# Performance work log

Measured on AMD Instinct MI355X. Metric: run time of the kernel, lower is better.

## Reference

```python
import jax, jax.numpy as jnp
import numpy as np

B, S, E, H = 4, 1024, 1024, 32
D = E // H  # head_dim == num_heads (required by phase broadcast in original code)


def setup_inputs() -> dict:
    key = jax.random.key(0)
    ks = jax.random.split(key, 20)
    s = 0.02
    inp = {
        "x": jax.random.normal(ks[0], (B, S, E), jnp.float32),
        # q/k/v projections (torch Linear: y = x @ W.T + b)
        "q_w": jax.random.normal(ks[1], (E, E), jnp.float32) * s,
        "q_b": jnp.zeros((E,), jnp.float32),
        "k_w": jax.random.normal(ks[2], (E, E), jnp.float32) * s,
        "k_b": jnp.zeros((E,), jnp.float32),
        "v_w": jax.random.normal(ks[3], (E, E), jnp.float32) * s,
        "v_b": jnp.zeros((E,), jnp.float32),
        # phase encoder: Linear(E,E) -> ReLU -> Linear(E,H)
        "ph_w1": jax.random.normal(ks[4], (E, E), jnp.float32) * s,
        "ph_b1": jnp.zeros((E,), jnp.float32),
        "ph_w2": jax.random.normal(ks[5], (H, E), jnp.float32) * s,
        "ph_b2": jnp.zeros((H,), jnp.float32),
        # nn.MultiheadAttention params (packed in_proj + out_proj)
        "in_proj_w": jax.random.normal(ks[6], (3 * E, E), jnp.float32) * s,
        "in_proj_b": jnp.zeros((3 * E,), jnp.float32),
        "out_proj_w": jax.random.normal(ks[7], (E, E), jnp.float32) * s,
        "out_proj_b": jnp.zeros((E,), jnp.float32),
        # final output projection
        "final_w": jax.random.normal(ks[8], (E, E), jnp.float32) * s,
        "final_b": jnp.zeros((E,), jnp.float32),
    }
    return inp


def _heads(t):  # (B,S,E) -> (B,H,S,D)
    return t.reshape(B, S, H, D).transpose(0, 2, 1, 3)


def _mha(x, in_proj_w, in_proj_b, out_proj_w, out_proj_b):
    # torch nn.MultiheadAttention self-attention, batch_first=True, no mask
    qkv = x @ in_proj_w.T + in_proj_b  # (B,S,3E)
    q, k, v = jnp.split(qkv, 3, axis=-1)
    q, k, v = _heads(q), _heads(k), _heads(v)
    scores = jnp.einsum("bhqd,bhkd->bhqk", q, k) / jnp.sqrt(jnp.float32(D))
    attn = jax.nn.softmax(scores, axis=-1)
    ctx = jnp.einsum("bhqk,bhkd->bhqd", attn, v)
    ctx = ctx.transpose(0, 2, 1, 3).reshape(B, S, E)
    return ctx @ out_proj_w.T + out_proj_b


def reference(x, q_w, q_b, k_w, k_b, v_w, v_b, ph_w1, ph_b1, ph_w2, ph_b2,
              in_proj_w, in_proj_b, out_proj_w, out_proj_b, final_w, final_b):
    Q = _heads(x @ q_w.T + q_b)  # (B,H,S,D)
    K = _heads(x @ k_w.T + k_b)
    V = _heads(x @ v_w.T + v_b)

    # phase: (B,H) -> cos -> broadcast over last (head_dim) axis, D == H
    h = jax.nn.relu(jnp.mean(x, axis=1) @ ph_w1.T + ph_b1)
    phase = jnp.cos(h @ ph_w2.T + ph_b2)  # (B,H)
    phase = phase[:, None, None, :]  # (B,1,1,H) multiplies head_dim axis

    Q = Q * phase
    K = K * phase
    scores = jnp.einsum("bhqd,bhkd->bhqk", Q, K) / jnp.sqrt(jnp.float32(D))
    attn_weights = jax.nn.softmax(scores, axis=-1)  # (B,H,S,S)
    context = jnp.einsum("bhqk,bhkd->bhqd", attn_weights, V)
    context = context.transpose(0, 2, 1, 3).reshape(B, S, E)

    entangled = _mha(context, in_proj_w, in_proj_b, out_proj_w, out_proj_b)
    output = (entangled + context) @ final_w.T + final_b
    return output, attn_weights
```

## Files before the change

### kernel.cpp

```cpp
#include <hip/hip_runtime.h>
#include <hip/hip_bf16.h>
#include <cstdint>
#include <cstddef>

typedef __bf16 bf16_t;
typedef __bf16 bf16x8 __attribute__((ext_vector_type(8)));
typedef __bf16 bf16x4 __attribute__((ext_vector_type(4)));
typedef float  f32x4  __attribute__((ext_vector_type(4)));

static constexpr int Bb = 4, Ss = 1024, Ee = 1024, Hh = 32, Dd = 32;
static constexpr int Ntok = Bb * Ss;
static constexpr int E3   = 3 * Ee;
static constexpr float SCALE = 0.17677669529663687f;

__device__ __forceinline__ void gl_lds16(const void* g, void* l) {
  __builtin_amdgcn_global_load_lds(
      (const __attribute__((address_space(1))) void*)g,
      (__attribute__((address_space(3))) void*)l, 16, 0, 0);
}

__global__ __launch_bounds__(256) void conv_all(const float* __restrict__ x,  const float* __restrict__ qw,
                                                const float* __restrict__ kw, const float* __restrict__ vw,
                                                const float* __restrict__ inw,const float* __restrict__ ow,
                                                const float* __restrict__ fw,
                                                bf16_t* xb, bf16_t* qb, bf16_t* kb, bf16_t* vb,
                                                bf16_t* inb, bf16_t* ob, bf16_t* fb) {
  const int i = blockIdx.x * 256 + threadIdx.x;
  const float* src; bf16_t* dst; int base;
  if      (i < 1048576) { src = x;   dst = xb;  base = 0; }
  else if (i < 1310720) { src = qw;  dst = qb;  base = 1048576; }
  else if (i < 1572864) { src = kw;  dst = kb;  base = 1310720; }
  else if (i < 1835008) { src = vw;  dst = vb;  base = 1572864; }
  else if (i < 2621440) { src = inw; dst = inb; base = 1835008; }
  else if (i < 2883584) { src = ow;  dst = ob;  base = 2621440; }
  else                  { src = fw;  dst = fb;  base = 2883584; }
  const int j = i - base;
  const float4 v = *(const float4*)(src + (size_t)j * 4);
  bf16x4 o = {(bf16_t)v.x, (bf16_t)v.y, (bf16_t)v.z, (bf16_t)v.w};
  *(bf16x4*)(dst + (size_t)j * 4) = o;
}

__global__ __launch_bounds__(256) void prepb(const float* __restrict__ qb, const float* __restrict__ kb,
                                             const float* __restrict__ vb, float* __restrict__ o) {
  const int i = blockIdx.x * 256 + threadIdx.x;
  o[i] = (i < 1024) ? qb[i] : (i < 2048) ? kb[i - 1024] : vb[i - 2048];
}

__global__ __launch_bounds__(256) void biasck(const float* __restrict__ fw, const float* __restrict__ ob,
                                              const float* __restrict__ fb, float* __restrict__ bc) {
  const int t = threadIdx.x;
  const int n = blockIdx.x * 64 + (t >> 2), p = t & 3;
  const float* row = fw + (size_t)n * 1024 + p * 256;
  const float* obp = ob + p * 256;
  float s = 0.f;
  for (int j = 0; j < 256; ++j) s += row[j] * obp[j];
  s += __shfl_xor(s, 1);
  s += __shfl_xor(s, 2);
  if (p == 0) bc[n] = s + fb[n];
}

__global__ __launch_bounds__(256) void colmean_part(const float* __restrict__ x,
                                                    float* __restrict__ part) {
  const int b = blockIdx.y, sc = blockIdx.x;
  const float* base = x + ((size_t)b * Ss + sc * 32) * Ee;
  for (int k = 0; k < 4; ++k) {
    const int e = threadIdx.x + k * 256;
    float s = 0.f;
    for (int i = 0; i < 32; ++i) s += base[(size_t)i * Ee + e];
    part[((size_t)sc * 4 + b) * Ee + e] = s;
  }
}
__global__ __launch_bounds__(256) void colmean_fin(const float* __restrict__ part,
                                                   float* __restrict__ xm) {
  const int idx = blockIdx.x * 256 + threadIdx.x;
  const int b = idx >> 10, e = idx & 1023;
  float s = 0.f;
  for (int sc = 0; sc < 32; ++sc) s += part[((size_t)sc * 4 + b) * Ee + e];
  xm[idx] = s * (1.0f / 1024.0f);
}

__global__ __launch_bounds__(256) void hgemm(const float* __restrict__ xm,
                                             const float* __restrict__ w1,
                                             const float* __restrict__ b1,
                                             float* __restrict__ hout) {
  __shared__ float xl[4 * 1024];
  for (int i = threadIdx.x; i < 4096; i += 256) xl[i] = xm[i];
  __syncthreads();
  const int j = blockIdx.x * 64 + (threadIdx.x >> 2);
  const int b = threadIdx.x & 3;
  const float* wr = w1 + (size_t)j * Ee;
  const float* xr = xl + b * 1024;
  float s = 0.f;
  for (int e = 0; e < 1024; ++e) s += xr[e] * wr[e];
  s += b1[j];
  hout[b * 1024 + j] = fmaxf(s, 0.f);
}

__global__ __launch_bounds__(128) void phasek(const float* __restrict__ hin,
                                              const float* __restrict__ w2,
                                              const float* __restrict__ b2,
                                              float* __restrict__ ph) {
  const int t = threadIdx.x;
  const int b = t >> 5, hh = t & 31;
  const float* hr = hin + b * 1024;
  const float* wr = w2 + (size_t)hh * Ee;
  float s = 0.f;
  for (int j = 0; j < 1024; ++j) s += hr[j] * wr[j];
  ph[t] = cosf(s + b2[hh]);
}

__global__ __launch_bounds__(256) void transpose1024(const bf16_t* __restrict__ in,
                                                     bf16_t* __restrict__ out) {
  __shared__ bf16_t t[64][72];
  const int jt = threadIdx.x >> 2, k16 = (threadIdx.x & 3) * 16;
  const int r0 = blockIdx.y * 64, c0 = blockIdx.x * 64;
  const bf16x8 a = *(const bf16x8*)(in + (size_t)(r0 + jt) * 1024 + c0 + k16);
  const bf16x8 b = *(const bf16x8*)(in + (size_t)(r0 + jt) * 1024 + c0 + k16 + 8);
  *(bf16x8*)&t[jt][k16] = a;
  *(bf16x8*)&t[jt][k16 + 8] = b;
  __syncthreads();
  bf16x8 v0, v1;
#pragma unroll
  for (int m = 0; m < 8; ++m) v0[m] = t[k16 + m][jt];
#pragma unroll
  for (int m = 0; m < 8; ++m) v1[m] = t[k16 + 8 + m][jt];
  *(bf16x8*)(out + (size_t)(c0 + jt) * 1024 + r0 + k16) = v0;
  *(bf16x8*)(out + (size_t)(c0 + jt) * 1024 + r0 + k16 + 8) = v1;
}

template <int MODE>
__global__ __launch_bounds__(256) void gemm_bt(const bf16_t* __restrict__ A,
                                               const bf16_t* __restrict__ A2,
                                               const bf16_t* __restrict__ Bt,
                                               const bf16_t* __restrict__ Bt2,
                                               const float* __restrict__ bias,
                                               void* __restrict__ Cout,
                                               const float* __restrict__ phase,
                                               int K, int lda, int ldb, int ldc) {
  __shared__ bf16_t As[128 * 32];
  __shared__ bf16_t Bs[128 * 32];
  const int tid = threadIdx.x;
  const int w = tid >> 6, lane = tid & 63;
  const int nwg = gridDim.x * gridDim.y;
  int flat = blockIdx.y * gridDim.x + blockIdx.x;
  flat = (flat & 7) * (nwg >> 3) + (flat >> 3);
  const int m0 = (flat / gridDim.x) * 128, n0 = (flat % gridDim.x) * 128;
  const int wr = (w >> 1) * 64, wc = (w & 1) * 64;
  const int r_ld = lane >> 2, c_ld = (lane & 3) * 8;
  const int rr = lane & 15, kk8 = (lane >> 4) * 8;
  f32x4 acc[4][4];
#pragma unroll
  for (int m = 0; m < 4; ++m)
#pragma unroll
    for (int n = 0; n < 4; ++n) acc[m][n] = f32x4{0.f, 0.f, 0.f, 0.f};

  for (int kt = 0; kt < K; kt += 32) {
    const bf16_t* Ak = A;
    const bf16_t* Bk = Bt;
    int kk = kt;
    if constexpr (MODE == 5) {
      if (kt >= 1024) { Ak = A2; Bk = Bt2; kk = kt - 1024; }
    }
#pragma unroll
    for (int j = 0; j < 2; ++j) {
      const int r0 = w * 16 + j * 64;
      gl_lds16(Ak + (size_t)(m0 + r0 + r_ld) * lda + kk + c_ld, &As[r0 * 32]);
      gl_lds16(Bk + (size_t)(n0 + r0 + r_ld) * ldb + kk + c_ld, &Bs[r0 * 32]);
    }
    __syncthreads();
    bf16x8 af[4], bfr[4];
#pragma unroll
    for (int m = 0; m < 4; ++m) af[m] = *(const bf16x8*)&As[(wr + m * 16 + rr) * 32 + kk8];
#pragma unroll
    for (int n = 0; n < 4; ++n) bfr[n] = *(const bf16x8*)&Bs[(wc + n * 16 + rr) * 32 + kk8];
#pragma unroll
    for (int m = 0; m < 4; ++m)
#pragma unroll
      for (int n = 0; n < 4; ++n)
        acc[m][n] = __builtin_amdgcn_mfma_f32_16x16x32_bf16(af[m], bfr[n], acc[m][n], 0, 0, 0);
    __syncthreads();
  }

  const int rr4 = (lane >> 4) * 4, cc = lane & 15;
#pragma unroll
  for (int m = 0; m < 4; ++m) {
#pragma unroll
    for (int n = 0; n < 4; ++n) {
      const int gr0 = m0 + wr + m * 16 + rr4;
      const int gc = n0 + wc + n * 16 + cc;
      const float bb = bias ? bias[gc] : 0.f;
#pragma unroll
      for (int i = 0; i < 4; ++i) {
        const size_t idx = (size_t)(gr0 + i) * ldc + gc;
        float v = acc[m][n][i] + bb;
        if constexpr (MODE == 4) {
          if (gc < 2048) v *= phase[(((gr0 + i) >> 10) << 5) + ((gc >> 5) & 31)];
        }
        if constexpr (MODE == 3 || MODE == 5) ((float*)Cout)[idx] = v;
        else ((bf16_t*)Cout)[idx] = (bf16_t)v;
      }
    }
  }
}

static constexpr int K_PLANE_B = 16400;
static constexpr int V_OFF_B   = 4 * K_PLANE_B;
static constexpr int V_ROW_B   = 2064;
static constexpr int P_OFF_B   = V_OFF_B + 32 * V_ROW_B;
static constexpr int P_WAVE_B  = 2304;
static constexpr int ATTN_LDS  = P_OFF_B + 8 * P_WAVE_B;

template <int WRITE_P>
__global__ __launch_bounds__(512) void attn_fused(const bf16_t* __restrict__ Qm,
                                                  const bf16_t* __restrict__ Km, int rs,
                                                  const bf16_t* __restrict__ Vt,
                                                  float* __restrict__ Pout,
                                                  bf16_t* __restrict__ ctx, float scale) {
  extern __shared__ char smem[];
  char* Kl = smem;
  char* Vl = smem + V_OFF_B;
  const int tid = threadIdx.x, lane = tid & 63, w = tid >> 6;
  const int g = lane >> 4, r = lane & 15;
  int flat = blockIdx.y * 8 + blockIdx.x;
  flat = (flat & 7) * 128 + (flat >> 3);
  const int bh = flat >> 3, xb = flat & 7;
  const int b = bh >> 5, h = bh & 31;
  char* myP = smem + P_OFF_B + w * P_WAVE_B;

  {
    const bf16_t* Kbase = Km + (size_t)b * Ss * rs + h * 32;
    const int pg = w >> 1, hh = w & 1;
#pragma unroll
    for (int c = 0; c < 8; ++c) {
      const int row0 = hh * 512 + c * 64;
      gl_lds16(Kbase + (size_t)(row0 + lane) * rs + pg * 8, Kl + pg * K_PLANE_B + row0 * 16);
    }
  }
  {
    const bf16_t* vsrc = Vt + (size_t)bh * (Dd * Ss);
#pragma unroll
    for (int rr2 = 0; rr2 < 4; ++rr2) {
      const int row = w * 4 + rr2;
#pragma unroll
      for (int c = 0; c < 2; ++c)
        gl_lds16(vsrc + (size_t)row * Ss + c * 512 + lane * 8, Vl + row * V_ROW_B + c * 1024);
    }
  }
  const int qrow0 = xb * 128 + w * 16;
  const bf16_t* Qbase = Qm + (size_t)b * Ss * rs + h * 32;
  const bf16x8 qraw = *(const bf16x8*)(Qbase + (size_t)(qrow0 + r) * rs + g * 8);
  bf16x8 qf;
#pragma unroll
  for (int i = 0; i < 8; ++i) qf[i] = (bf16_t)((float)qraw[i] * scale);
  __syncthreads();

  const f32x4 zero = {0.f, 0.f, 0.f, 0.f};
  float lsum = 0.f;
  float rinv = 1.f;

  if constexpr (WRITE_P) {
    for (int kt = 0; kt < 16; ++kt) {
#pragma unroll
      for (int n = 0; n < 4; ++n) {
        const int key = kt * 64 + n * 16 + r;
        const bf16x8 kf = *(const bf16x8*)(Kl + g * K_PLANE_B + key * 16);
        const f32x4 s = __builtin_amdgcn_mfma_f32_16x16x32_bf16(kf, qf, zero, 0, 0, 0);
#pragma unroll
        for (int i = 0; i < 4; ++i) lsum += __expf(fminf(s[i], 60.f));
      }
    }
    lsum += __shfl_xor(lsum, 16);
    lsum += __shfl_xor(lsum, 32);
    rinv = 1.0f / lsum;
  }

  f32x4 acc2[2] = {zero, zero};
  const size_t pbase = (size_t)bh * Ss * Ss;

  for (int kt = 0; kt < 16; ++kt) {
    float p[4][4];
#pragma unroll
    for (int n = 0; n < 4; ++n) {
      const int key = kt * 64 + n * 16 + r;
      const bf16x8 kf = *(const bf16x8*)(Kl + g * K_PLANE_B + key * 16);
      const f32x4 s = __builtin_amdgcn_mfma_f32_16x16x32_bf16(kf, qf, zero, 0, 0, 0);
#pragma unroll
      for (int i = 0; i < 4; ++i) {
        float e = __expf(fminf(s[i], 60.f));
        if constexpr (WRITE_P) e *= rinv;
        else lsum += e;
        p[n][i] = e;
      }
      bf16x4 pw = {(bf16_t)p[n][0], (bf16_t)p[n][1], (bf16_t)p[n][2], (bf16_t)p[n][3]};
      *(bf16x4*)(myP + r * 144 + (n * 16 + g * 4) * 2) = pw;
      if constexpr (WRITE_P) {
        f32x4 w4 = {p[n][0], p[n][1], p[n][2], p[n][3]};
        *(f32x4*)&Pout[pbase + (size_t)(qrow0 + r) * Ss + kt * 64 + n * 16 + 4 * g] = w4;
      }
    }
#pragma unroll
    for (int c = 0; c < 2; ++c) {
      const bf16x8 pa = *(const bf16x8*)(myP + r * 144 + (c * 32 + 8 * g) * 2);
#pragma unroll
      for (int dn = 0; dn < 2; ++dn) {
        const bf16x8 vf = *(const bf16x8*)(Vl + (dn * 16 + r) * V_ROW_B +
                                           (kt * 64 + c * 32 + g * 8) * 2);
        acc2[dn] = __builtin_amdgcn_mfma_f32_16x16x32_bf16(vf, pa, acc2[dn], 0, 0, 0);
      }
    }
  }

  if constexpr (!WRITE_P) {
    lsum += __shfl_xor(lsum, 16);
    lsum += __shfl_xor(lsum, 32);
    rinv = 1.0f / lsum;
#pragma unroll
    for (int dn = 0; dn < 2; ++dn)
#pragma unroll
      for (int i = 0; i < 4; ++i) acc2[dn][i] *= rinv;
  }

  float* Ct = (float*)myP;
#pragma unroll
  for (int dn = 0; dn < 2; ++dn)
#pragma unroll
    for (int i = 0; i < 4; ++i)
      Ct[r * 36 + dn * 16 + 4 * g + i] = acc2[dn][i];
  const int q2 = lane >> 2, pt = lane & 3;
  const f32x4 ca = *(const f32x4*)(myP + q2 * 144 + pt * 32);
  const f32x4 cb = *(const f32x4*)(myP + q2 * 144 + pt * 32 + 16);
  bf16x8 cv = {(bf16_t)ca[0], (bf16_t)ca[1], (bf16_t)ca[2], (bf16_t)ca[3],
               (bf16_t)cb[0], (bf16_t)cb[1], (bf16_t)cb[2], (bf16_t)cb[3]};
  *(bf16x8*)&ctx[((size_t)b * Ss + qrow0 + q2) * Ee + h * 32 + pt * 8] = cv;
}

__global__ __launch_bounds__(256) void transpose_v(const bf16_t* __restrict__ src, int rs,
                                                   bf16_t* __restrict__ dst) {
  __shared__ bf16_t buf[128 * 33];
  const int bh = blockIdx.y, b = bh >> 5, h = bh & 31;
  const int s0 = blockIdx.x * 128;
  const bf16_t* in = src + ((size_t)b * Ss + s0) * rs + h * 32;
  for (int e = threadIdx.x; e < 128 * 32; e += 256) {
    const int s = e >> 5, d = e & 31;
    buf[s * 33 + d] = in[(size_t)s * rs + d];
  }
  __syncthreads();
  bf16_t* out = dst + (size_t)bh * (Dd * Ss) + s0;
  for (int e = threadIdx.x; e < 128 * 32; e += 256) {
    const int d = e >> 7, s = e & 127;
    out[(size_t)d * Ss + s] = buf[s * 33 + d];
  }
}

extern "C" void kernel_launch(void* const* d_in, const int* in_sizes, int n_in,
                              void* d_out, int out_size, void* d_ws, size_t ws_size,
                              hipStream_t stream) {
  const float* x     = (const float*)d_in[0];
  const float* q_w   = (const float*)d_in[1];
  const float* q_b   = (const float*)d_in[2];
  const float* k_w   = (const float*)d_in[3];
  const float* k_b   = (const float*)d_in[4];
  const float* v_w   = (const float*)d_in[5];
  const float* v_b   = (const float*)d_in[6];
  const float* ph_w1 = (const float*)d_in[7];
  const float* ph_b1 = (const float*)d_in[8];
  const float* ph_w2 = (const float*)d_in[9];
  const float* ph_b2 = (const float*)d_in[10];
  const float* in_w  = (const float*)d_in[11];
  const float* in_b  = (const float*)d_in[12];
  const float* out_w = (const float*)d_in[13];
  const float* out_b = (const float*)d_in[14];
  const float* fin_w = (const float*)d_in[15];
  const float* fin_b = (const float*)d_in[16];

  float* outp = (float*)d_out;
  float* attn_out = outp + (size_t)Ntok * Ee;

  char* ws = (char*)d_ws;
  size_t off = 0;
  auto alloc = [&](size_t bytes) -> void* {
    void* p = ws + off;
    off += (bytes + 255) & ~(size_t)255;
    return p;
  };
  bf16_t* x_bf  = (bf16_t*)alloc((size_t)Ntok * Ee * 2);
  bf16_t* wqkv  = (bf16_t*)alloc((size_t)E3 * Ee * 2);
  bf16_t* win   = (bf16_t*)alloc((size_t)E3 * Ee * 2);
  bf16_t* wout  = (bf16_t*)alloc((size_t)Ee * Ee * 2);
  bf16_t* wfin  = (bf16_t*)alloc((size_t)Ee * Ee * 2);
  bf16_t* woutT = (bf16_t*)alloc((size_t)Ee * Ee * 2);
  bf16_t* Wc    = (bf16_t*)alloc((size_t)Ee * Ee * 2);
  bf16_t* QKVb  = (bf16_t*)alloc((size_t)Ntok * E3 * 2);
  bf16_t* Vt    = (bf16_t*)alloc((size_t)Bb * Hh * Dd * Ss * 2);
  bf16_t* ctx   = (bf16_t*)alloc((size_t)Ntok * Ee * 2);
  bf16_t* qkv2  = (bf16_t*)alloc((size_t)Ntok * E3 * 2);
  bf16_t* v2t   = (bf16_t*)alloc((size_t)Bb * Hh * Dd * Ss * 2);
  bf16_t* ctx2  = (bf16_t*)alloc((size_t)Ntok * Ee * 2);
  float* part   = (float*)alloc((size_t)32 * 4 * 1024 * 4);
  float* xmean  = (float*)alloc(4096 * 4);
  float* hb     = (float*)alloc(4096 * 4);
  float* phase  = (float*)alloc(128 * 4);
  float* qkvb   = (float*)alloc(3072 * 4);
  float* bias_c = (float*)alloc(1024 * 4);

  hipFuncSetAttribute((const void*)attn_fused<1>,
                      hipFuncAttributeMaxDynamicSharedMemorySize, ATTN_LDS);
  hipFuncSetAttribute((const void*)attn_fused<0>,
                      hipFuncAttributeMaxDynamicSharedMemorySize, ATTN_LDS);

  conv_all<<<12288, 256, 0, stream>>>(x, q_w, k_w, v_w, in_w, out_w, fin_w,
                                      x_bf, wqkv, wqkv + (size_t)Ee * Ee,
                                      wqkv + (size_t)2 * Ee * Ee, win, wout, wfin);
  prepb<<<12, 256, 0, stream>>>(q_b, k_b, v_b, qkvb);
  biasck<<<16, 256, 0, stream>>>(fin_w, out_b, fin_b, bias_c);

  colmean_part<<<dim3(32, 4), 256, 0, stream>>>(x, part);
  colmean_fin<<<16, 256, 0, stream>>>(part, xmean);
  hgemm<<<16, 256, 0, stream>>>(xmean, ph_w1, ph_b1, hb);
  phasek<<<1, 128, 0, stream>>>(hb, ph_w2, ph_b2, phase);

  transpose1024<<<dim3(16, 16), 256, 0, stream>>>(wout, woutT);
  gemm_bt<0><<<dim3(8, 8), 256, 0, stream>>>(wfin, nullptr, woutT, nullptr, nullptr,
                                             Wc, nullptr, 1024, Ee, Ee, Ee);

  gemm_bt<4><<<dim3(24, 32), 256, 0, stream>>>(x_bf, nullptr, wqkv, nullptr, qkvb,
                                               QKVb, phase, 1024, Ee, Ee, E3);
  transpose_v<<<dim3(8, 128), 256, 0, stream>>>(QKVb + 2048, E3, Vt);

  attn_fused<1><<<dim3(8, 128), 512, ATTN_LDS, stream>>>(QKVb, QKVb + 1024, E3, Vt,
                                                         attn_out, ctx, SCALE);

  gemm_bt<0><<<dim3(24, 32), 256, 0, stream>>>(ctx, nullptr, win, nullptr, in_b,
                                               qkv2, nullptr, 1024, Ee, Ee, E3);
  transpose_v<<<dim3(8, 128), 256, 0, stream>>>(qkv2 + 2048, E3, v2t);
  attn_fused<0><<<dim3(8, 128), 512, ATTN_LDS, stream>>>(qkv2, qkv2 + 1024, E3, v2t,
                                                         nullptr, ctx2, SCALE);

  gemm_bt<5><<<dim3(8, 32), 256, 0, stream>>>(ctx2, ctx, Wc, wfin, bias_c,
                                              outp, nullptr, 2048, Ee, Ee, Ee);
}
```

Before: 542.2 us.

## Fuse prep kernels, reorganize K into MFMA-fragment layout, swizzle LDS, use exp2

Result: slower. 718.5 us (+32.5%).

```diff
diff --git a/kernel.cpp b/kernel.cpp
--- a/kernel.cpp
+++ b/kernel.cpp
@@ -11,7 +11,8 @@
 static constexpr int Bb = 4, Ss = 1024, Ee = 1024, Hh = 32, Dd = 32;
 static constexpr int Ntok = Bb * Ss;
 static constexpr int E3   = 3 * Ee;
-static constexpr float SCALE = 0.17677669529663687f;
+static constexpr float SCALE  = 0.17677669529663687f;
+static constexpr float SCALE2 = 0.25506060570135506f;
 
 __device__ __forceinline__ void gl_lds16(const void* g, void* l) {
   __builtin_amdgcn_global_load_lds(
@@ -19,94 +20,99 @@
       (__attribute__((address_space(3))) void*)l, 16, 0, 0);
 }
 
-__global__ __launch_bounds__(256) void conv_all(const float* __restrict__ x,  const float* __restrict__ qw,
-                                                const float* __restrict__ kw, const float* __restrict__ vw,
-                                                const float* __restrict__ inw,const float* __restrict__ ow,
-                                                const float* __restrict__ fw,
-                                                bf16_t* xb, bf16_t* qb, bf16_t* kb, bf16_t* vb,
-                                                bf16_t* inb, bf16_t* ob, bf16_t* fb) {
-  const int i = blockIdx.x * 256 + threadIdx.x;
-  const float* src; bf16_t* dst; int base;
-  if      (i < 1048576) { src = x;   dst = xb;  base = 0; }
-  else if (i < 1310720) { src = qw;  dst = qb;  base = 1048576; }
-  else if (i < 1572864) { src = kw;  dst = kb;  base = 1310720; }
-  else if (i < 1835008) { src = vw;  dst = vb;  base = 1572864; }
-  else if (i < 2621440) { src = inw; dst = inb; base = 1835008; }
-  else if (i < 2883584) { src = ow;  dst = ob;  base = 2621440; }
-  else                  { src = fw;  dst = fb;  base = 2883584; }
-  const int j = i - base;
-  const float4 v = *(const float4*)(src + (size_t)j * 4);
-  bf16x4 o = {(bf16_t)v.x, (bf16_t)v.y, (bf16_t)v.z, (bf16_t)v.w};
-  *(bf16x4*)(dst + (size_t)j * 4) = o;
-}
-
-__global__ __launch_bounds__(256) void prepb(const float* __restrict__ qb, const float* __restrict__ kb,
-                                             const float* __restrict__ vb, float* __restrict__ o) {
-  const int i = blockIdx.x * 256 + threadIdx.x;
-  o[i] = (i < 1024) ? qb[i] : (i < 2048) ? kb[i - 1024] : vb[i - 2048];
-}
-
-__global__ __launch_bounds__(256) void biasck(const float* __restrict__ fw, const float* __restrict__ ob,
-                                              const float* __restrict__ fb, float* __restrict__ bc) {
+__global__ __launch_bounds__(256) void prep(const float* __restrict__ x,  const float* __restrict__ qw,
+                                            const float* __restrict__ kw, const float* __restrict__ vw,
+                                            const float* __restrict__ inw,const float* __restrict__ ow,
+                                            const float* __restrict__ fw,
+                                            const float* __restrict__ qb, const float* __restrict__ kb,
+                                            const float* __restrict__ vb, const float* __restrict__ ob,
+                                            const float* __restrict__ fb,
+                                            bf16_t* __restrict__ xb, bf16_t* __restrict__ wqkv,
+                                            bf16_t* __restrict__ winb, bf16_t* __restrict__ wob,
+                                            bf16_t* __restrict__ wfb,
+                                            float* __restrict__ qkvb, float* __restrict__ bias_c,
+                                            float* __restrict__ part) {
+  const int bx = blockIdx.x, t = threadIdx.x;
+  if (bx < 12288) {
+    const int i = bx * 256 + t;
+    const float* src; bf16_t* dst; int base;
+    if      (i < 1048576) { src = x;   dst = xb;                       base = 0; }
+    else if (i < 1310720) { src = qw;  dst = wqkv;                     base = 1048576; }
+    else if (i < 1572864) { src = kw;  dst = wqkv + (size_t)Ee * Ee;   base = 1310720; }
+    else if (i < 1835008) { src = vw;  dst = wqkv + (size_t)2*Ee*Ee;   base = 1572864; }
+    else if (i < 2621440) { src = inw; dst = winb;                     base = 1835008; }
+    else if (i < 2883584) { src = ow;  dst = wob;                      base = 2621440; }
+    else                  { src = fw;  dst = wfb;                      base = 2883584; }
+    const int j = i - base;
+    const float4 v = *(const float4*)(src + (size_t)j * 4);
+    bf16x4 o = {(bf16_t)v.x, (bf16_t)v.y, (bf16_t)v.z, (bf16_t)v.w};
+    *(bf16x4*)(dst + (size_t)j * 4) = o;
+  } else if (bx < 12300) {
+    const int i = (bx - 12288) * 256 + t;
+    qkvb[i] = (i < 1024) ? qb[i] : (i < 2048) ? kb[i - 1024] : vb[i - 2048];
+  } else if (bx < 12316) {
+    const int n = (bx - 12300) * 64 + (t >> 2), p = t & 3;
+    const float* row = fw + (size_t)n * 1024 + p * 256;
+    const float* obp = ob + p * 256;
+    float s = 0.f;
+    for (int j = 0; j < 256; ++j) s += row[j] * obp[j];
+    s += __shfl_xor(s, 1);
+    s += __shfl_xor(s, 2);
+    if (p == 0) bias_c[n] = s + fb[n];
+  } else {
+    const int idx = bx - 12316;
+    const int sc = idx & 31, b = idx >> 5;
+    const float* base = x + ((size_t)b * Ss + sc * 32) * Ee;
+    for (int k = 0; k < 4; ++k) {
+      const int e = t + k * 256;
+      float s = 0.f;
+      for (int i = 0; i < 32; ++i) s += base[(size_t)i * Ee + e];
+      part[((size_t)sc * 4 + b) * Ee + e] = s;
+    }
+  }
+}
+
+__global__ __launch_bounds__(1024) void phase_fin(const float* __restrict__ part,
+                                                  const float* __restrict__ w1,
+                                                  const float* __restrict__ b1,
+                                                  const float* __restrict__ w2,
+                                                  const float* __restrict__ b2,
+                                                  float* __restrict__ phase) {
+  __shared__ float xm[4096];
+  __shared__ float hb[4096];
   const int t = threadIdx.x;
-  const int n = blockIdx.x * 64 + (t >> 2), p = t & 3;
-  const float* row = fw + (size_t)n * 1024 + p * 256;
-  const float* obp = ob + p * 256;
-  float s = 0.f;
-  for (int j = 0; j < 256; ++j) s += row[j] * obp[j];
-  s += __shfl_xor(s, 1);
-  s += __shfl_xor(s, 2);
-  if (p == 0) bc[n] = s + fb[n];
-}
-
-__global__ __launch_bounds__(256) void colmean_part(const float* __restrict__ x,
-                                                    float* __restrict__ part) {
-  const int b = blockIdx.y, sc = blockIdx.x;
-  const float* base = x + ((size_t)b * Ss + sc * 32) * Ee;
-  for (int k = 0; k < 4; ++k) {
-    const int e = threadIdx.x + k * 256;
+#pragma unroll
+  for (int j = 0; j < 4; ++j) {
+    const int idx = t + j * 1024;
+    const int b = idx >> 10, e = idx & 1023;
     float s = 0.f;
-    for (int i = 0; i < 32; ++i) s += base[(size_t)i * Ee + e];
-    part[((size_t)sc * 4 + b) * Ee + e] = s;
-  }
-}
-__global__ __launch_bounds__(256) void colmean_fin(const float* __restrict__ part,
-                                                   float* __restrict__ xm) {
-  const int idx = blockIdx.x * 256 + threadIdx.x;
-  const int b = idx >> 10, e = idx & 1023;
-  float s = 0.f;
-  for (int sc = 0; sc < 32; ++sc) s += part[((size_t)sc * 4 + b) * Ee + e];
-  xm[idx] = s * (1.0f / 1024.0f);
-}
-
-__global__ __launch_bounds__(256) void hgemm(const float* __restrict__ xm,
-                                             const float* __restrict__ w1,
-                                             const float* __restrict__ b1,
-                                             float* __restrict__ hout) {
-  __shared__ float xl[4 * 1024];
-  for (int i = threadIdx.x; i < 4096; i += 256) xl[i] = xm[i];
+    for (int sc = 0; sc < 32; ++sc) s += part[((size_t)sc * 4 + b) * 1024 + e];
+    xm[idx] = s * (1.0f / 1024.0f);
+  }
   __syncthreads();
-  const int j = blockIdx.x * 64 + (threadIdx.x >> 2);
-  const int b = threadIdx.x & 3;
-  const float* wr = w1 + (size_t)j * Ee;
-  const float* xr = xl + b * 1024;
-  float s = 0.f;
-  for (int e = 0; e < 1024; ++e) s += xr[e] * wr[e];
-  s += b1[j];
-  hout[b * 1024 + j] = fmaxf(s, 0.f);
-}
-
-__global__ __launch_bounds__(128) void phasek(const float* __restrict__ hin,
-                                              const float* __restrict__ w2,
-                                              const float* __restrict__ b2,
-                                              float* __restrict__ ph) {
-  const int t = threadIdx.x;
-  const int b = t >> 5, hh = t & 31;
-  const float* hr = hin + b * 1024;
-  const float* wr = w2 + (size_t)hh * Ee;
-  float s = 0.f;
-  for (int j = 0; j < 1024; ++j) s += hr[j] * wr[j];
-  ph[t] = cosf(s + b2[hh]);
+  {
+    const float* wr = w1 + (size_t)t * 1024;
+    float a0 = 0.f, a1 = 0.f, a2 = 0.f, a3 = 0.f;
+    for (int e = 0; e < 1024; ++e) {
+      const float wv = wr[e];
+      a0 += xm[e] * wv; a1 += xm[1024 + e] * wv;
+      a2 += xm[2048 + e] * wv; a3 += xm[3072 + e] * wv;
+    }
+    const float bb = b1[t];
+    hb[t]        = fmaxf(a0 + bb, 0.f);
+    hb[1024 + t] = fmaxf(a1 + bb, 0.f);
+    hb[2048 + t] = fmaxf(a2 + bb, 0.f);
+    hb[3072 + t] = fmaxf(a3 + bb, 0.f);
+  }
+  __syncthreads();
+  if (t < 128) {
+    const int b = t >> 5, hh = t & 31;
+    const float* hr = hb + b * 1024;
+    const float* wr = w2 + (size_t)hh * 1024;
+    float s = 0.f;
+    for (int j = 0; j < 1024; ++j) s += hr[j] * wr[j];
+    phase[t] = cosf(s + b2[hh]);
+  }
 }
 
 __global__ __launch_bounds__(256) void transpose1024(const bf16_t* __restrict__ in,
@@ -196,83 +202,98 @@
         if constexpr (MODE == 4) {
           if (gc < 2048) v *= phase[(((gr0 + i) >> 10) << 5) + ((gc >> 5) & 31)];
         }
-        if constexpr (MODE == 3 || MODE == 5) ((float*)Cout)[idx] = v;
+        if constexpr (MODE == 5) ((float*)Cout)[idx] = v;
         else ((bf16_t*)Cout)[idx] = (bf16_t)v;
       }
     }
   }
 }
 
-static constexpr int K_PLANE_B = 16400;
-static constexpr int V_OFF_B   = 4 * K_PLANE_B;
-static constexpr int V_ROW_B   = 2064;
-static constexpr int P_OFF_B   = V_OFF_B + 32 * V_ROW_B;
-static constexpr int P_WAVE_B  = 2304;
-static constexpr int ATTN_LDS  = P_OFF_B + 8 * P_WAVE_B;
+__global__ __launch_bounds__(256) void reorg_kv(const bf16_t* __restrict__ Ksrc,
+                                                const bf16_t* __restrict__ Vsrc, int rs,
+                                                bf16_t* __restrict__ K2,
+                                                bf16_t* __restrict__ Vt) {
+  const int bh = blockIdx.y, b = bh >> 5, h = bh & 31;
+  if (blockIdx.x < 8) {
+    __shared__ bf16_t buf[128 * 33];
+    const int s0 = blockIdx.x * 128;
+    const bf16_t* in = Vsrc + ((size_t)b * Ss + s0) * rs + h * 32;
+    for (int e = threadIdx.x; e < 128 * 32; e += 256) {
+      const int s = e >> 5, d = e & 31;
+      buf[s * 33 + d] = in[(size_t)s * rs + d];
+    }
+    __syncthreads();
+    bf16_t* outp = Vt + (size_t)bh * 32768 + s0;
+    for (int e = threadIdx.x; e < 128 * 32; e += 256) {
+      const int d = e >> 7, s = e & 127;
+      outp[(size_t)d * 1024 + s] = buf[s * 33 + d];
+    }
+  } else {
+    const int xx = blockIdx.x - 8;
+    const int idx = xx * 2048 + threadIdx.x * 8;
+    const int kt = idx >> 11, rem = idx & 2047;
+    const int n = rem >> 9, rem2 = rem & 511;
+    const int r = rem2 >> 5, g = (rem2 >> 3) & 3;
+    const int s = kt * 64 + n * 16 + r;
+    const bf16x8 v = *(const bf16x8*)(Ksrc + ((size_t)b * Ss + s) * rs + h * 32 + g * 8);
+    *(bf16x8*)(K2 + (size_t)bh * 32768 + idx) = v;
+  }
+}
+
+static constexpr int ATTN_LDS = 81920;
 
 template <int WRITE_P>
-__global__ __launch_bounds__(512) void attn_fused(const bf16_t* __restrict__ Qm,
-                                                  const bf16_t* __restrict__ Km, int rs,
+__global__ __launch_bounds__(512) void attn_fused(const bf16_t* __restrict__ Qm, int rs,
+                                                  const bf16_t* __restrict__ K2,
                                                   const bf16_t* __restrict__ Vt,
                                                   float* __restrict__ Pout,
-                                                  bf16_t* __restrict__ ctx, float scale) {
+                                                  bf16_t* __restrict__ ctx, float scale2) {
   extern __shared__ char smem[];
-  char* Kl = smem;
-  char* Vl = smem + V_OFF_B;
+  char* Vl = smem;
   const int tid = threadIdx.x, lane = tid & 63, w = tid >> 6;
-  const int g = lane >> 4, r = lane & 15;
+  const int g = lane >> 4, r = lane & 15, rx = r & 7;
+  char* myP = smem + 65536 + w * 2048;
   int flat = blockIdx.y * 8 + blockIdx.x;
   flat = (flat & 7) * 128 + (flat >> 3);
   const int bh = flat >> 3, xb = flat & 7;
   const int b = bh >> 5, h = bh & 31;
-  char* myP = smem + P_OFF_B + w * P_WAVE_B;
 
   {
-    const bf16_t* Kbase = Km + (size_t)b * Ss * rs + h * 32;
-    const int pg = w >> 1, hh = w & 1;
-#pragma unroll
-    for (int c = 0; c < 8; ++c) {
-      const int row0 = hh * 512 + c * 64;
-      gl_lds16(Kbase + (size_t)(row0 + lane) * rs + pg * 8, Kl + pg * K_PLANE_B + row0 * 16);
-    }
-  }
-  {
-    const bf16_t* vsrc = Vt + (size_t)bh * (Dd * Ss);
+    const bf16_t* vsrc = Vt + (size_t)bh * 32768;
 #pragma unroll
     for (int rr2 = 0; rr2 < 4; ++rr2) {
-      const int row = w * 4 + rr2;
+      const int d = w * 4 + rr2;
 #pragma unroll
       for (int c = 0; c < 2; ++c)
-        gl_lds16(vsrc + (size_t)row * Ss + c * 512 + lane * 8, Vl + row * V_ROW_B + c * 1024);
+        gl_lds16(vsrc + d * 1024 + (((c * 64 + lane) ^ (d & 7)) * 8), Vl + d * 2048 + c * 1024);
     }
   }
   const int qrow0 = xb * 128 + w * 16;
-  const bf16_t* Qbase = Qm + (size_t)b * Ss * rs + h * 32;
-  const bf16x8 qraw = *(const bf16x8*)(Qbase + (size_t)(qrow0 + r) * rs + g * 8);
+  const bf16x8 qraw = *(const bf16x8*)(Qm + ((size_t)b * Ss + qrow0 + r) * rs + h * 32 + g * 8);
   bf16x8 qf;
 #pragma unroll
-  for (int i = 0; i < 8; ++i) qf[i] = (bf16_t)((float)qraw[i] * scale);
-  __syncthreads();
-
+  for (int i = 0; i < 8; ++i) qf[i] = (bf16_t)((float)qraw[i] * scale2);
+
+  const bf16_t* k2 = K2 + (size_t)bh * 32768;
+  const int koff = r * 32 + g * 8;
   const f32x4 zero = {0.f, 0.f, 0.f, 0.f};
-  float lsum = 0.f;
-  float rinv = 1.f;
+  float lsum = 0.f, rinv = 1.f;
 
   if constexpr (WRITE_P) {
     for (int kt = 0; kt < 16; ++kt) {
 #pragma unroll
       for (int n = 0; n < 4; ++n) {
-        const int key = kt * 64 + n * 16 + r;
-        const bf16x8 kf = *(const bf16x8*)(Kl + g * K_PLANE_B + key * 16);
+        const bf16x8 kf = *(const bf16x8*)(k2 + (kt * 4 + n) * 512 + koff);
         const f32x4 s = __builtin_amdgcn_mfma_f32_16x16x32_bf16(kf, qf, zero, 0, 0, 0);
 #pragma unroll
-        for (int i = 0; i < 4; ++i) lsum += __expf(fminf(s[i], 60.f));
+        for (int i = 0; i < 4; ++i) lsum += exp2f(fminf(s[i], 80.f));
       }
     }
     lsum += __shfl_xor(lsum, 16);
     lsum += __shfl_xor(lsum, 32);
     rinv = 1.0f / lsum;
   }
+  __syncthreads();
 
   f32x4 acc2[2] = {zero, zero};
   const size_t pbase = (size_t)bh * Ss * Ss;
@@ -281,18 +302,17 @@
     float p[4][4];
 #pragma unroll
     for (int n = 0; n < 4; ++n) {
-      const int key = kt * 64 + n * 16 + r;
-      const bf16x8 kf = *(const bf16x8*)(Kl + g * K_PLANE_B + key * 16);
+      const bf16x8 kf = *(const bf16x8*)(k2 + (kt * 4 + n) * 512 + koff);
       const f32x4 s = __builtin_amdgcn_mfma_f32_16x16x32_bf16(kf, qf, zero, 0, 0, 0);
 #pragma unroll
       for (int i = 0; i < 4; ++i) {
-        float e = __expf(fminf(s[i], 60.f));
+        float e = exp2f(fminf(s[i], 80.f));
         if constexpr (WRITE_P) e *= rinv;
         else lsum += e;
         p[n][i] = e;
       }
       bf16x4 pw = {(bf16_t)p[n][0], (bf16_t)p[n][1], (bf16_t)p[n][2], (bf16_t)p[n][3]};
-      *(bf16x4*)(myP + r * 144 + (n * 16 + g * 4) * 2) = pw;
+      *(bf16x4*)(myP + r * 128 + (((2 * n + (g >> 1)) ^ rx) << 4) + ((g & 1) << 3)) = pw;
       if constexpr (WRITE_P) {
         f32x4 w4 = {p[n][0], p[n][1], p[n][2], p[n][3]};
         *(f32x4*)&Pout[pbase + (size_t)(qrow0 + r) * Ss + kt * 64 + n * 16 + 4 * g] = w4;
@@ -300,11 +320,11 @@
     }
 #pragma unroll
     for (int c = 0; c < 2; ++c) {
-      const bf16x8 pa = *(const bf16x8*)(myP + r * 144 + (c * 32 + 8 * g) * 2);
+      const bf16x8 pa = *(const bf16x8*)(myP + r * 128 + (((4 * c + g) ^ rx) << 4));
 #pragma unroll
       for (int dn = 0; dn < 2; ++dn) {
-        const bf16x8 vf = *(const bf16x8*)(Vl + (dn * 16 + r) * V_ROW_B +
-                                           (kt * 64 + c * 32 + g * 8) * 2);
+        const int d = dn * 16 + r;
+        const bf16x8 vf = *(const bf16x8*)(Vl + d * 2048 + (((kt * 8 + c * 4 + g) ^ rx) << 4));
         acc2[dn] = __builtin_amdgcn_mfma_f32_16x16x32_bf16(vf, pa, acc2[dn], 0, 0, 0);
       }
     }
@@ -314,41 +334,14 @@
     lsum += __shfl_xor(lsum, 16);
     lsum += __shfl_xor(lsum, 32);
     rinv = 1.0f / lsum;
-#pragma unroll
-    for (int dn = 0; dn < 2; ++dn)
-#pragma unroll
-      for (int i = 0; i < 4; ++i) acc2[dn][i] *= rinv;
-  }
-
-  float* Ct = (float*)myP;
-#pragma unroll
-  for (int dn = 0; dn < 2; ++dn)
+  }
+#pragma unroll
+  for (int dn = 0; dn < 2; ++dn) {
+    bf16x4 cv;
 #pragma unroll
     for (int i = 0; i < 4; ++i)
-      Ct[r * 36 + dn * 16 + 4 * g + i] = acc2[dn][i];
-  const int q2 = lane >> 2, pt = lane & 3;
-  const f32x4 ca = *(const f32x4*)(myP + q2 * 144 + pt * 32);
-  const f32x4 cb = *(const f32x4*)(myP + q2 * 144 + pt * 32 + 16);
-  bf16x8 cv = {(bf16_t)ca[0], (bf16_t)ca[1], (bf16_t)ca[2], (bf16_t)ca[3],
-               (bf16_t)cb[0], (bf16_t)cb[1], (bf16_t)cb[2], (bf16_t)cb[3]};
-  *(bf16x8*)&ctx[((size_t)b * Ss + qrow0 + q2) * Ee + h * 32 + pt * 8] = cv;
-}
-
-__global__ __launch_bounds__(256) void transpose_v(const bf16_t* __restrict__ src, int rs,
-                                                   bf16_t* __restrict__ dst) {
-  __shared__ bf16_t buf[128 * 33];
-  const int bh = blockIdx.y, b = bh >> 5, h = bh & 31;
-  const int s0 = blockIdx.x * 128;
-  const bf16_t* in = src + ((size_t)b * Ss + s0) * rs + h * 32;
-  for (int e = threadIdx.x; e < 128 * 32; e += 256) {
-    const int s = e >> 5, d = e & 31;
-    buf[s * 33 + d] = in[(size_t)s * rs + d];
-  }
-  __syncthreads();
-  bf16_t* out = dst + (size_t)bh * (Dd * Ss) + s0;
-  for (int e = threadIdx.x; e < 128 * 32; e += 256) {
-    const int d = e >> 7, s = e & 127;
-    out[(size_t)d * Ss + s] = buf[s * 33 + d];
+      cv[i] = (bf16_t)(WRITE_P ? acc2[dn][i] : acc2[dn][i] * rinv);
+    *(bf16x4*)&ctx[((size_t)b * Ss + qrow0 + r) * Ee + h * 32 + dn * 16 + 4 * g] = cv;
   }
 }
 
@@ -391,14 +384,14 @@
   bf16_t* woutT = (bf16_t*)alloc((size_t)Ee * Ee * 2);
   bf16_t* Wc    = (bf16_t*)alloc((size_t)Ee * Ee * 2);
   bf16_t* QKVb  = (bf16_t*)alloc((size_t)Ntok * E3 * 2);
-  bf16_t* Vt    = (bf16_t*)alloc((size_t)Bb * Hh * Dd * Ss * 2);
+  bf16_t* Vt    = (bf16_t*)alloc((size_t)128 * 32768 * 2);
+  bf16_t* K2a   = (bf16_t*)alloc((size_t)128 * 32768 * 2);
   bf16_t* ctx   = (bf16_t*)alloc((size_t)Ntok * Ee * 2);
   bf16_t* qkv2  = (bf16_t*)alloc((size_t)Ntok * E3 * 2);
-  bf16_t* v2t   = (bf16_t*)alloc((size_t)Bb * Hh * Dd * Ss * 2);
+  bf16_t* v2t   = (bf16_t*)alloc((size_t)128 * 32768 * 2);
+  bf16_t* K2b   = (bf16_t*)alloc((size_t)128 * 32768 * 2);
   bf16_t* ctx2  = (bf16_t*)alloc((size_t)Ntok * Ee * 2);
   float* part   = (float*)alloc((size_t)32 * 4 * 1024 * 4);
-  float* xmean  = (float*)alloc(4096 * 4);
-  float* hb     = (float*)alloc(4096 * 4);
   float* phase  = (float*)alloc(128 * 4);
   float* qkvb   = (float*)alloc(3072 * 4);
   float* bias_c = (float*)alloc(1024 * 4);
@@ -408,34 +401,23 @@
   hipFuncSetAttribute((const void*)attn_fused<0>,
                       hipFuncAttributeMaxDynamicSharedMemorySize, ATTN_LDS);
 
-  conv_all<<<12288, 256, 0, stream>>>(x, q_w, k_w, v_w, in_w, out_w, fin_w,
-                                      x_bf, wqkv, wqkv + (size_t)Ee * Ee,
-                                      wqkv + (size_t)2 * Ee * Ee, win, wout, wfin);
-  prepb<<<12, 256, 0, stream>>>(q_b, k_b, v_b, qkvb);
-  biasck<<<16, 256, 0, stream>>>(fin_w, out_b, fin_b, bias_c);
-
-  colmean_part<<<dim3(32, 4), 256, 0, stream>>>(x, part);
-  colmean_fin<<<16, 256, 0, stream>>>(part, xmean);
-  hgemm<<<16, 256, 0, stream>>>(xmean, ph_w1, ph_b1, hb);
-  phasek<<<1, 128, 0, stream>>>(hb, ph_w2, ph_b2, phase);
-
+  prep<<<12444, 256, 0, stream>>>(x, q_w, k_w, v_w, in_w, out_w, fin_w,
+                                  q_b, k_b, v_b, out_b, fin_b,
+                                  x_bf, wqkv, win, wout, wfin, qkvb, bias_c, part);
+  phase_fin<<<1, 1024, 0, stream>>>(part, ph_w1, ph_b1, ph_w2, ph_b2, phase);
   transpose1024<<<dim3(16, 16), 256, 0, stream>>>(wout, woutT);
   gemm_bt<0><<<dim3(8, 8), 256, 0, stream>>>(wfin, nullptr, woutT, nullptr, nullptr,
                                              Wc, nullptr, 1024, Ee, Ee, Ee);
-
   gemm_bt<4><<<dim3(24, 32), 256, 0, stream>>>(x_bf, nullptr, wqkv, nullptr, qkvb,
                                                QKVb, phase, 1024, Ee, Ee, E3);
-  transpose_v<<<dim3(8, 128), 256, 0, stream>>>(QKVb + 2048, E3, Vt);
-
-  attn_fused<1><<<dim3(8, 128), 512, ATTN_LDS, stream>>>(QKVb, QKVb + 1024, E3, Vt,
-                                                         attn_out, ctx, SCALE);
-
+  reorg_kv<<<dim3(24, 128), 256, 0, stream>>>(QKVb + 1024, QKVb + 2048, E3, K2a, Vt);
+  attn_fused<1><<<dim3(8, 128), 512, ATTN_LDS, stream>>>(QKVb, E3, K2a, Vt,
+                                                         attn_out, ctx, SCALE2);
   gemm_bt<0><<<dim3(24, 32), 256, 0, stream>>>(ctx, nullptr, win, nullptr, in_b,
                                                qkv2, nullptr, 1024, Ee, Ee, E3);
-  transpose_v<<<dim3(8, 128), 256, 0, stream>>>(qkv2 + 2048, E3, v2t);
-  attn_fused<0><<<dim3(8, 128), 512, ATTN_LDS, stream>>>(qkv2, qkv2 + 1024, E3, v2t,
-                                                         nullptr, ctx2, SCALE);
-
+  reorg_kv<<<dim3(24, 128), 256, 0, stream>>>(qkv2 + 1024, qkv2 + 2048, E3, K2b, v2t);
+  attn_fused<0><<<dim3(8, 128), 512, ATTN_LDS, stream>>>(qkv2, E3, K2b, v2t,
+                                                         nullptr, ctx2, SCALE2);
   gemm_bt<5><<<dim3(8, 32), 256, 0, stream>>>(ctx2, ctx, Wc, wfin, bias_c,
                                               outp, nullptr, 2048, Ee, Ee, Ee);
 }
```
